# Kernel optimization log

Measured on AMD Instinct MI355X. Metric: run time of the kernel, lower is better.

Reference implementation:

```python
import jax, jax.numpy as jnp
import numpy as np

SIZE = 2.0            # scene extent, matches init size
N_LEVELS = 16         # Instant-NGP default
TABLE_SIZE = 1 << 19  # hash entries per level (power of 2)
FEAT = 2              # embedding_length per level
BASE_RES = 16         # init resolution
MAX_RES = 2048
N_POINTS = 1 << 21

_OFFS = np.array([[(c >> d) & 1 for d in range(3)] for c in range(8)])  # [8,3] corner bits
_PRIMES = np.array([1, 2654435761, 805459861], dtype=np.uint32)         # NGP spatial hash primes


def setup_inputs() -> dict:
    key = jax.random.key(0)
    k1, k2 = jax.random.split(key)
    xyz = (jax.random.uniform(k1, (N_POINTS, 3), dtype=jnp.float32) - 0.5) * SIZE
    tables = jax.random.normal(k2, (N_LEVELS, TABLE_SIZE, FEAT), dtype=jnp.float32) * 1e-2
    # geometric resolution schedule 16 -> 2048 over 16 levels
    growth = (MAX_RES / BASE_RES) ** (np.arange(N_LEVELS) / (N_LEVELS - 1))
    resolutions = jnp.asarray(np.floor(BASE_RES * growth).astype(np.int32))
    return {"xyz": xyz, "tables": tables, "resolutions": resolutions}


def _encode(xyz, tables, resolutions):
    u = xyz / SIZE + 0.5                              # [N,3] in [0,1)
    offs_u = jnp.asarray(_OFFS.astype(np.uint32))     # [8,3]
    offs_f = jnp.asarray(_OFFS.astype(np.float32))    # [8,3]
    primes = jnp.asarray(_PRIMES)

    def level(_, xs):
        table, res = xs                               # [T,F], scalar int32
        p = u * res.astype(jnp.float32)               # [N,3]
        p0 = jnp.floor(p)
        w = p - p0                                    # trilinear fractions [N,3]
        c = p0.astype(jnp.uint32)[:, None, :] + offs_u[None]     # [N,8,3]
        h = (c[..., 0] * primes[0]) ^ (c[..., 1] * primes[1]) ^ (c[..., 2] * primes[2])
        idx = (h & jnp.uint32(TABLE_SIZE - 1)).astype(jnp.int32)  # [N,8]
        feats = table[idx]                                        # [N,8,F] gather
        wc = jnp.prod(jnp.where(offs_f[None] > 0, w[:, None, :], 1.0 - w[:, None, :]), axis=-1)  # [N,8]
        return None, jnp.sum(feats * wc[..., None], axis=1)      # [N,F]

    _, embs = jax.lax.scan(level, None, (tables, resolutions))   # [L,N,F]
    n = xyz.shape[0]
    return jnp.transpose(embs, (1, 0, 2)).reshape(n, N_LEVELS * FEAT)


def reference(xyz, tables, resolutions):
    return _encode(xyz, tables, resolutions)
```

## Files before the change

### kernel.cpp

```cpp
#include <hip/hip_runtime.h>
#include <hip/hip_fp16.h>

#define NLV 16
#define TBL (1u << 19)
#define TMASK (TBL - 1u)
#define P1 2654435761u
#define P2 805459861u
#define NBIN (1 << 18)

typedef float vf2 __attribute__((ext_vector_type(2)));
typedef float vf4 __attribute__((ext_vector_type(4)));
typedef unsigned vu2 __attribute__((ext_vector_type(2)));

__device__ __forceinline__ vf2 h2_to_f2(unsigned bits) {
    union { unsigned u; __half2 h; } c; c.u = bits;
    float2 f = __half22float2(c.h);
    vf2 r; r.x = f.x; r.y = f.y; return r;
}
__device__ __forceinline__ unsigned f2_to_h2(float a, float b) {
    union { __half2 h; unsigned u; } c; c.h = __floats2half2_rn(a, b);
    return c.u;
}

__device__ __forceinline__ unsigned mort6(unsigned v) {
    v &= 63u;
    v = (v | (v << 16)) & 0x030000FFu;
    v = (v | (v << 8))  & 0x0300F00Fu;
    v = (v | (v << 4))  & 0x030C30C3u;
    v = (v | (v << 2))  & 0x09249249u;
    return v;
}

__device__ __forceinline__ unsigned bin_of(float ux, float uy, float uz) {
    unsigned bx = min(63u, (unsigned)(ux * 64.0f));
    unsigned by = min(63u, (unsigned)(uy * 64.0f));
    unsigned bz = min(63u, (unsigned)(uz * 64.0f));
    return mort6(bx) | (mort6(by) << 1) | (mort6(bz) << 2);
}

__global__ __launch_bounds__(256) void convert_tables(
    const float* __restrict__ tables, unsigned* __restrict__ htab, int total)
{
    int i = blockIdx.x * 256 + threadIdx.x;
    int e0 = i * 2;
    if (e0 >= total) return;
    vf4 v = *(const vf4*)(tables + (size_t)e0 * 2);
    vu2 o; o.x = f2_to_h2(v.x, v.y); o.y = f2_to_h2(v.z, v.w);
    *(vu2*)(htab + e0) = o;
}

__global__ __launch_bounds__(256) void hist_kernel(
    const float* __restrict__ xyz, unsigned* __restrict__ hist, int n)
{
    int p = blockIdx.x * 256 + threadIdx.x;
    if (p >= n) return;
    float ux = xyz[(size_t)p * 3 + 0] * 0.5f + 0.5f;
    float uy = xyz[(size_t)p * 3 + 1] * 0.5f + 0.5f;
    float uz = xyz[(size_t)p * 3 + 2] * 0.5f + 0.5f;
    atomicAdd(&hist[bin_of(ux, uy, uz)], 1u);
}

__global__ __launch_bounds__(1024) void scan_bins(unsigned* __restrict__ hist)
{
    __shared__ unsigned part[1024];
    int t = threadIdx.x;
    int base = t * (NBIN / 1024);
    unsigned s = 0;
    for (int j = 0; j < NBIN / 1024; ++j) s += hist[base + j];
    part[t] = s;
    __syncthreads();
    for (int off = 1; off < 1024; off <<= 1) {
        unsigned v = (t >= off) ? part[t - off] : 0u;
        __syncthreads();
        part[t] += v;
        __syncthreads();
    }
    unsigned run = (t == 0) ? 0u : part[t - 1];
    for (int j = 0; j < NBIN / 1024; ++j) {
        unsigned tmp = hist[base + j];
        hist[base + j] = run;
        run += tmp;
    }
}

__global__ __launch_bounds__(256) void scatter_kernel(
    const float* __restrict__ xyz, unsigned* __restrict__ start,
    vf4* __restrict__ u4s, int* __restrict__ orig, int n)
{
    int p = blockIdx.x * 256 + threadIdx.x;
    if (p >= n) return;
    float ux = xyz[(size_t)p * 3 + 0] * 0.5f + 0.5f;
    float uy = xyz[(size_t)p * 3 + 1] * 0.5f + 0.5f;
    float uz = xyz[(size_t)p * 3 + 2] * 0.5f + 0.5f;
    unsigned pos = atomicAdd(&start[bin_of(ux, uy, uz)], 1u);
    orig[pos] = p;
    vf4 r; r.x = ux; r.y = uy; r.z = uz; r.w = 0.0f;
    u4s[pos] = r;
}

__global__ __launch_bounds__(256) void ngp_gather_s(
    const vf4* __restrict__ u4s,
    const unsigned* __restrict__ htab,
    const int* __restrict__ resolutions,
    unsigned* __restrict__ wsout,
    int n, int nbPerLevel)
{
    int L = blockIdx.x / nbPerLevel;
    int chunk = blockIdx.x % nbPerLevel;
    int p0 = chunk * 1024 + (int)threadIdx.x;

    float res = (float)resolutions[L];
    const unsigned* __restrict__ tab = htab + (size_t)L * TBL;
    unsigned* __restrict__ wl = wsout + (size_t)L * n;

    unsigned idx[4][8];
    float wx[4], wyz[4][4];
    bool valid[4];

#pragma unroll
    for (int q = 0; q < 4; ++q) {
        int p = p0 + q * 256;
        valid[q] = (p < n);
        int pp = valid[q] ? p : 0;
        vf4 u = u4s[pp];
        float px = u.x * res, py = u.y * res, pz = u.z * res;
        float fx = floorf(px), fy = floorf(py), fz = floorf(pz);
        float wxl = px - fx, wyl = py - fy, wzl = pz - fz;
        unsigned cx = (unsigned)fx, cy = (unsigned)fy, cz = (unsigned)fz;
        unsigned hx0 = cx, hx1 = cx + 1u;
        unsigned hy0 = cy * P1, hy1 = hy0 + P1;
        unsigned hz0 = cz * P2, hz1 = hz0 + P2;
#pragma unroll
        for (int c = 0; c < 8; ++c)
            idx[q][c] = ((((c & 1) ? hx1 : hx0) ^
                          ((c & 2) ? hy1 : hy0) ^
                          ((c & 4) ? hz1 : hz0)) & TMASK);
        float vy = 1.0f - wyl, vz = 1.0f - wzl;
        wx[q] = wxl;
        wyz[q][0] = vy * vz;  wyz[q][1] = wyl * vz;
        wyz[q][2] = vy * wzl; wyz[q][3] = wyl * wzl;
    }

    unsigned d[4][8];
#pragma unroll
    for (int q = 0; q < 4; ++q)
#pragma unroll
        for (int c = 0; c < 8; ++c)
            d[q][c] = tab[idx[q][c]];

#pragma unroll
    for (int q = 0; q < 4; ++q) {
        float vx = 1.0f - wx[q];
        float a0 = 0.0f, a1 = 0.0f;
#pragma unroll
        for (int c = 0; c < 8; ++c) {
            float w = wyz[q][c >> 1] * ((c & 1) ? wx[q] : vx);
            vf2 f = h2_to_f2(d[q][c]);
            a0 += f.x * w;
            a1 += f.y * w;
        }
        int p = p0 + q * 256;
        if (valid[q]) wl[p] = f2_to_h2(a0, a1);
    }
}

__global__ __launch_bounds__(256) void ngp_finalize_s(
    const unsigned* __restrict__ ws, const int* __restrict__ orig,
    float* __restrict__ out, int n)
{
    int i = blockIdx.x * 256 + threadIdx.x;
    if (i >= n) return;
    int op = orig[i];
    vf4* o = (vf4*)(out + (size_t)op * (NLV * 2));
#pragma unroll
    for (int j = 0; j < 8; ++j) {
        vf2 ga = h2_to_f2(ws[(size_t)(2 * j) * n + i]);
        vf2 gb = h2_to_f2(ws[(size_t)(2 * j + 1) * n + i]);
        vf4 r; r.x = ga.x; r.y = ga.y; r.z = gb.x; r.w = gb.y;
        o[j] = r;
    }
}

__global__ __launch_bounds__(256) void ngp_encode_kernel(
    const float* __restrict__ xyz,
    const float* __restrict__ tables,
    const int* __restrict__ resolutions,
    float* __restrict__ out,
    int n)
{
    int p = blockIdx.x * blockDim.x + threadIdx.x;
    if (p >= n) return;

    float x = xyz[(size_t)p * 3 + 0];
    float y = xyz[(size_t)p * 3 + 1];
    float z = xyz[(size_t)p * 3 + 2];
    float ux = x * 0.5f + 0.5f;
    float uy = y * 0.5f + 0.5f;
    float uz = z * 0.5f + 0.5f;

    float acc[NLV * 2];

#pragma unroll
    for (int L = 0; L < NLV; ++L) {
        float res = (float)resolutions[L];
        float px = ux * res, py = uy * res, pz = uz * res;
        float fx = floorf(px), fy = floorf(py), fz = floorf(pz);
        float wx = px - fx, wy = py - fy, wz = pz - fz;
        unsigned cx = (unsigned)fx, cy = (unsigned)fy, cz = (unsigned)fz;
        unsigned hx0 = cx, hx1 = cx + 1u;
        unsigned hy0 = cy * P1, hy1 = hy0 + P1;
        unsigned hz0 = cz * P2, hz1 = hz0 + P2;
        const vf2* __restrict__ tab = (const vf2*)tables + (size_t)L * TBL;
        float vx = 1.0f - wx, vy = 1.0f - wy, vz = 1.0f - wz;
        float a0 = 0.0f, a1 = 0.0f;
#pragma unroll
        for (int c = 0; c < 8; ++c) {
            unsigned h = ((c & 1) ? hx1 : hx0) ^
                         ((c & 2) ? hy1 : hy0) ^
                         ((c & 4) ? hz1 : hz0);
            vf2 f = tab[h & TMASK];
            float w = ((c & 1) ? wx : vx) *
                      ((c & 2) ? wy : vy) *
                      ((c & 4) ? wz : vz);
            a0 += f.x * w;
            a1 += f.y * w;
        }
        acc[L * 2 + 0] = a0;
        acc[L * 2 + 1] = a1;
    }

    vf4* o = (vf4*)(out + (size_t)p * (NLV * 2));
#pragma unroll
    for (int i = 0; i < 8; ++i) {
        vf4 r; r.x = acc[i * 4 + 0]; r.y = acc[i * 4 + 1];
        r.z = acc[i * 4 + 2]; r.w = acc[i * 4 + 3];
        o[i] = r;
    }
}

extern "C" void kernel_launch(void* const* d_in, const int* in_sizes, int n_in,
                              void* d_out, int out_size, void* d_ws, size_t ws_size,
                              hipStream_t stream) {
    const float* xyz = (const float*)d_in[0];
    const float* tables = (const float*)d_in[1];
    const int* resolutions = (const int*)d_in[2];
    float* out = (float*)d_out;

    int n = in_sizes[0] / 3;
    const int totalEntries = NLV * (int)TBL;

    const size_t tabBytes  = (size_t)totalEntries * 4;
    const size_t u4Bytes   = (size_t)n * sizeof(vf4);
    const size_t origBytes = (size_t)n * 4;
    const size_t histBytes = (size_t)NBIN * 4;
    const size_t wsoutBytes = (size_t)NLV * (size_t)n * 4;
    const size_t need = tabBytes + u4Bytes + origBytes + histBytes + wsoutBytes;

    if (ws_size >= need) {
        char* base = (char*)d_ws;
        unsigned* htab  = (unsigned*)base;                       base += tabBytes;
        vf4*      u4s   = (vf4*)base;                            base += u4Bytes;
        int*      orig  = (int*)base;                            base += origBytes;
        unsigned* hist  = (unsigned*)base;                       base += histBytes;
        unsigned* wsout = (unsigned*)base;

        hipMemsetAsync(hist, 0, histBytes, stream);

        int gridC = (totalEntries / 2 + 255) / 256;
        hipLaunchKernelGGL(convert_tables, dim3(gridC), dim3(256), 0, stream,
                           tables, htab, totalEntries);

        int gridP = (n + 255) / 256;
        hipLaunchKernelGGL(hist_kernel, dim3(gridP), dim3(256), 0, stream,
                           xyz, hist, n);
        hipLaunchKernelGGL(scan_bins, dim3(1), dim3(1024), 0, stream, hist);
        hipLaunchKernelGGL(scatter_kernel, dim3(gridP), dim3(256), 0, stream,
                           xyz, hist, u4s, orig, n);

        int nbPerLevel = (n + 1023) / 1024;
        int grid1 = NLV * nbPerLevel;
        hipLaunchKernelGGL(ngp_gather_s, dim3(grid1), dim3(256), 0, stream,
                           u4s, htab, resolutions, wsout, n, nbPerLevel);

        hipLaunchKernelGGL(ngp_finalize_s, dim3(gridP), dim3(256), 0, stream,
                           wsout, orig, out, n);
    } else {
        int grid = (n + 255) / 256;
        hipLaunchKernelGGL(ngp_encode_kernel, dim3(grid), dim3(256), 0, stream,
                           xyz, tables, resolutions, out, n);
    }
}
```

Baseline: 884.2 us.

## Fuse per-level gather with finalize, coarsen Morton bins, vectorize hist/scatter

Replaces the level-major gather kernel plus separate finalize pass with one point-major kernel that walks all 16 levels, two at a time, per point and writes the output row directly. This drops the fp16 intermediate workspace and its write/read round trip. Morton sort bins shrink from 64^3 to 32^3, and the histogram and scatter kernels now process four points per thread using vector loads. The trade-off is that fine levels no longer get level-major scheduling, so table locality in cache may be worse.

```diff
diff --git a/kernel.cpp b/kernel.cpp
--- a/kernel.cpp
+++ b/kernel.cpp
@@ -6,7 +6,7 @@
 #define TMASK (TBL - 1u)
 #define P1 2654435761u
 #define P2 805459861u
-#define NBIN (1 << 18)
+#define NBIN (1 << 15)
 
 typedef float vf2 __attribute__((ext_vector_type(2)));
 typedef float vf4 __attribute__((ext_vector_type(4)));
@@ -22,8 +22,8 @@
     return c.u;
 }
 
-__device__ __forceinline__ unsigned mort6(unsigned v) {
-    v &= 63u;
+__device__ __forceinline__ unsigned mort5(unsigned v) {
+    v &= 31u;
     v = (v | (v << 16)) & 0x030000FFu;
     v = (v | (v << 8))  & 0x0300F00Fu;
     v = (v | (v << 4))  & 0x030C30C3u;
@@ -32,10 +32,10 @@
 }
 
 __device__ __forceinline__ unsigned bin_of(float ux, float uy, float uz) {
-    unsigned bx = min(63u, (unsigned)(ux * 64.0f));
-    unsigned by = min(63u, (unsigned)(uy * 64.0f));
-    unsigned bz = min(63u, (unsigned)(uz * 64.0f));
-    return mort6(bx) | (mort6(by) << 1) | (mort6(bz) << 2);
+    unsigned bx = min(31u, (unsigned)(ux * 32.0f));
+    unsigned by = min(31u, (unsigned)(uy * 32.0f));
+    unsigned bz = min(31u, (unsigned)(uz * 32.0f));
+    return mort5(bx) | (mort5(by) << 1) | (mort5(bz) << 2);
 }
 
 __global__ __launch_bounds__(256) void convert_tables(
@@ -52,12 +52,25 @@
 __global__ __launch_bounds__(256) void hist_kernel(
     const float* __restrict__ xyz, unsigned* __restrict__ hist, int n)
 {
-    int p = blockIdx.x * 256 + threadIdx.x;
+    int t = blockIdx.x * 256 + threadIdx.x;
+    int p = t * 4;
     if (p >= n) return;
-    float ux = xyz[(size_t)p * 3 + 0] * 0.5f + 0.5f;
-    float uy = xyz[(size_t)p * 3 + 1] * 0.5f + 0.5f;
-    float uz = xyz[(size_t)p * 3 + 2] * 0.5f + 0.5f;
-    atomicAdd(&hist[bin_of(ux, uy, uz)], 1u);
+    if (p + 3 < n) {
+        vf4 a = *(const vf4*)(xyz + (size_t)p * 3);
+        vf4 b = *(const vf4*)(xyz + (size_t)p * 3 + 4);
+        vf4 c = *(const vf4*)(xyz + (size_t)p * 3 + 8);
+        atomicAdd(&hist[bin_of(a.x*0.5f+0.5f, a.y*0.5f+0.5f, a.z*0.5f+0.5f)], 1u);
+        atomicAdd(&hist[bin_of(a.w*0.5f+0.5f, b.x*0.5f+0.5f, b.y*0.5f+0.5f)], 1u);
+        atomicAdd(&hist[bin_of(b.z*0.5f+0.5f, b.w*0.5f+0.5f, c.x*0.5f+0.5f)], 1u);
+        atomicAdd(&hist[bin_of(c.y*0.5f+0.5f, c.z*0.5f+0.5f, c.w*0.5f+0.5f)], 1u);
+    } else {
+        for (int q = 0; q < 4 && p + q < n; ++q) {
+            float ux = xyz[(size_t)(p+q)*3+0]*0.5f+0.5f;
+            float uy = xyz[(size_t)(p+q)*3+1]*0.5f+0.5f;
+            float uz = xyz[(size_t)(p+q)*3+2]*0.5f+0.5f;
+            atomicAdd(&hist[bin_of(ux,uy,uz)], 1u);
+        }
+    }
 }
 
 __global__ __launch_bounds__(1024) void scan_bins(unsigned* __restrict__ hist)
@@ -87,96 +100,108 @@
     const float* __restrict__ xyz, unsigned* __restrict__ start,
     vf4* __restrict__ u4s, int* __restrict__ orig, int n)
 {
-    int p = blockIdx.x * 256 + threadIdx.x;
+    int t = blockIdx.x * 256 + threadIdx.x;
+    int p = t * 4;
     if (p >= n) return;
-    float ux = xyz[(size_t)p * 3 + 0] * 0.5f + 0.5f;
-    float uy = xyz[(size_t)p * 3 + 1] * 0.5f + 0.5f;
-    float uz = xyz[(size_t)p * 3 + 2] * 0.5f + 0.5f;
-    unsigned pos = atomicAdd(&start[bin_of(ux, uy, uz)], 1u);
-    orig[pos] = p;
-    vf4 r; r.x = ux; r.y = uy; r.z = uz; r.w = 0.0f;
-    u4s[pos] = r;
-}
-
-__global__ __launch_bounds__(256) void ngp_gather_s(
+    float U[4][3];
+    int cnt = (p + 3 < n) ? 4 : (n - p);
+    if (cnt == 4) {
+        vf4 a = *(const vf4*)(xyz + (size_t)p * 3);
+        vf4 b = *(const vf4*)(xyz + (size_t)p * 3 + 4);
+        vf4 c = *(const vf4*)(xyz + (size_t)p * 3 + 8);
+        U[0][0]=a.x; U[0][1]=a.y; U[0][2]=a.z;
+        U[1][0]=a.w; U[1][1]=b.x; U[1][2]=b.y;
+        U[2][0]=b.z; U[2][1]=b.w; U[2][2]=c.x;
+        U[3][0]=c.y; U[3][1]=c.z; U[3][2]=c.w;
+    } else {
+        for (int q = 0; q < cnt; ++q) {
+            U[q][0]=xyz[(size_t)(p+q)*3+0];
+            U[q][1]=xyz[(size_t)(p+q)*3+1];
+            U[q][2]=xyz[(size_t)(p+q)*3+2];
+        }
+    }
+#pragma unroll
+    for (int q = 0; q < 4; ++q) {
+        if (q >= cnt) break;
+        float ux = U[q][0]*0.5f+0.5f, uy = U[q][1]*0.5f+0.5f, uz = U[q][2]*0.5f+0.5f;
+        unsigned pos = atomicAdd(&start[bin_of(ux,uy,uz)], 1u);
+        orig[pos] = p + q;
+        vf4 r; r.x = ux; r.y = uy; r.z = uz; r.w = 0.0f;
+        u4s[pos] = r;
+    }
+}
+
+__global__ __launch_bounds__(256) void ngp_fused(
     const vf4* __restrict__ u4s,
     const unsigned* __restrict__ htab,
     const int* __restrict__ resolutions,
-    unsigned* __restrict__ wsout,
-    int n, int nbPerLevel)
-{
-    int L = blockIdx.x / nbPerLevel;
-    int chunk = blockIdx.x % nbPerLevel;
-    int p0 = chunk * 1024 + (int)threadIdx.x;
-
-    float res = (float)resolutions[L];
-    const unsigned* __restrict__ tab = htab + (size_t)L * TBL;
-    unsigned* __restrict__ wl = wsout + (size_t)L * n;
-
-    unsigned idx[4][8];
-    float wx[4], wyz[4][4];
-    bool valid[4];
-
-#pragma unroll
-    for (int q = 0; q < 4; ++q) {
-        int p = p0 + q * 256;
-        valid[q] = (p < n);
-        int pp = valid[q] ? p : 0;
-        vf4 u = u4s[pp];
-        float px = u.x * res, py = u.y * res, pz = u.z * res;
-        float fx = floorf(px), fy = floorf(py), fz = floorf(pz);
-        float wxl = px - fx, wyl = py - fy, wzl = pz - fz;
-        unsigned cx = (unsigned)fx, cy = (unsigned)fy, cz = (unsigned)fz;
-        unsigned hx0 = cx, hx1 = cx + 1u;
-        unsigned hy0 = cy * P1, hy1 = hy0 + P1;
-        unsigned hz0 = cz * P2, hz1 = hz0 + P2;
-#pragma unroll
-        for (int c = 0; c < 8; ++c)
-            idx[q][c] = ((((c & 1) ? hx1 : hx0) ^
-                          ((c & 2) ? hy1 : hy0) ^
-                          ((c & 4) ? hz1 : hz0)) & TMASK);
-        float vy = 1.0f - wyl, vz = 1.0f - wzl;
-        wx[q] = wxl;
-        wyz[q][0] = vy * vz;  wyz[q][1] = wyl * vz;
-        wyz[q][2] = vy * wzl; wyz[q][3] = wyl * wzl;
-    }
-
-    unsigned d[4][8];
-#pragma unroll
-    for (int q = 0; q < 4; ++q)
-#pragma unroll
-        for (int c = 0; c < 8; ++c)
-            d[q][c] = tab[idx[q][c]];
-
-#pragma unroll
-    for (int q = 0; q < 4; ++q) {
-        float vx = 1.0f - wx[q];
-        float a0 = 0.0f, a1 = 0.0f;
-#pragma unroll
-        for (int c = 0; c < 8; ++c) {
-            float w = wyz[q][c >> 1] * ((c & 1) ? wx[q] : vx);
-            vf2 f = h2_to_f2(d[q][c]);
-            a0 += f.x * w;
-            a1 += f.y * w;
-        }
-        int p = p0 + q * 256;
-        if (valid[q]) wl[p] = f2_to_h2(a0, a1);
-    }
-}
-
-__global__ __launch_bounds__(256) void ngp_finalize_s(
-    const unsigned* __restrict__ ws, const int* __restrict__ orig,
+    const int* __restrict__ orig,
     float* __restrict__ out, int n)
 {
     int i = blockIdx.x * 256 + threadIdx.x;
     if (i >= n) return;
+
+    vf4 u = u4s[i];
     int op = orig[i];
+
+    float acc[NLV * 2];
+
+#pragma unroll
+    for (int Lp = 0; Lp < NLV / 2; ++Lp) {
+        unsigned idx[2][8];
+        float wxs[2], wyz[2][4];
+#pragma unroll
+        for (int s = 0; s < 2; ++s) {
+            int L = 2 * Lp + s;
+            float res = (float)resolutions[L];
+            float px = u.x * res, py = u.y * res, pz = u.z * res;
+            float fx = floorf(px), fy = floorf(py), fz = floorf(pz);
+            float wxl = px - fx, wyl = py - fy, wzl = pz - fz;
+            unsigned cx = (unsigned)fx, cy = (unsigned)fy, cz = (unsigned)fz;
+            unsigned hx0 = cx, hx1 = cx + 1u;
+            unsigned hy0 = cy * P1, hy1 = hy0 + P1;
+            unsigned hz0 = cz * P2, hz1 = hz0 + P2;
+#pragma unroll
+            for (int c = 0; c < 8; ++c)
+                idx[s][c] = ((((c & 1) ? hx1 : hx0) ^
+                              ((c & 2) ? hy1 : hy0) ^
+                              ((c & 4) ? hz1 : hz0)) & TMASK);
+            float vy = 1.0f - wyl, vz = 1.0f - wzl;
+            wxs[s] = wxl;
+            wyz[s][0] = vy * vz;  wyz[s][1] = wyl * vz;
+            wyz[s][2] = vy * wzl; wyz[s][3] = wyl * wzl;
+        }
+
+        unsigned d[2][8];
+#pragma unroll
+        for (int s = 0; s < 2; ++s) {
+            const unsigned* __restrict__ tab = htab + (size_t)(2 * Lp + s) * TBL;
+#pragma unroll
+            for (int c = 0; c < 8; ++c)
+                d[s][c] = tab[idx[s][c]];
+        }
+
+#pragma unroll
+        for (int s = 0; s < 2; ++s) {
+            float vx = 1.0f - wxs[s];
+            float a0 = 0.0f, a1 = 0.0f;
+#pragma unroll
+            for (int c = 0; c < 8; ++c) {
+                float w = wyz[s][c >> 1] * ((c & 1) ? wxs[s] : vx);
+                vf2 f = h2_to_f2(d[s][c]);
+                a0 += f.x * w;
+                a1 += f.y * w;
+            }
+            acc[(2 * Lp + s) * 2 + 0] = a0;
+            acc[(2 * Lp + s) * 2 + 1] = a1;
+        }
+    }
+
     vf4* o = (vf4*)(out + (size_t)op * (NLV * 2));
 #pragma unroll
     for (int j = 0; j < 8; ++j) {
-        vf2 ga = h2_to_f2(ws[(size_t)(2 * j) * n + i]);
-        vf2 gb = h2_to_f2(ws[(size_t)(2 * j + 1) * n + i]);
-        vf4 r; r.x = ga.x; r.y = ga.y; r.z = gb.x; r.w = gb.y;
+        vf4 r; r.x = acc[j * 4 + 0]; r.y = acc[j * 4 + 1];
+        r.z = acc[j * 4 + 2]; r.w = acc[j * 4 + 3];
         o[j] = r;
     }
 }
@@ -253,16 +278,14 @@
     const size_t u4Bytes   = (size_t)n * sizeof(vf4);
     const size_t origBytes = (size_t)n * 4;
     const size_t histBytes = (size_t)NBIN * 4;
-    const size_t wsoutBytes = (size_t)NLV * (size_t)n * 4;
-    const size_t need = tabBytes + u4Bytes + origBytes + histBytes + wsoutBytes;
+    const size_t need = tabBytes + u4Bytes + origBytes + histBytes;
 
     if (ws_size >= need) {
         char* base = (char*)d_ws;
         unsigned* htab  = (unsigned*)base;                       base += tabBytes;
         vf4*      u4s   = (vf4*)base;                            base += u4Bytes;
         int*      orig  = (int*)base;                            base += origBytes;
-        unsigned* hist  = (unsigned*)base;                       base += histBytes;
-        unsigned* wsout = (unsigned*)base;
+        unsigned* hist  = (unsigned*)base;
 
         hipMemsetAsync(hist, 0, histBytes, stream);
 
@@ -270,20 +293,16 @@
         hipLaunchKernelGGL(convert_tables, dim3(gridC), dim3(256), 0, stream,
                            tables, htab, totalEntries);
 
-        int gridP = (n + 255) / 256;
-        hipLaunchKernelGGL(hist_kernel, dim3(gridP), dim3(256), 0, stream,
+        int grid4 = ((n + 3) / 4 + 255) / 256;
+        hipLaunchKernelGGL(hist_kernel, dim3(grid4), dim3(256), 0, stream,
                            xyz, hist, n);
         hipLaunchKernelGGL(scan_bins, dim3(1), dim3(1024), 0, stream, hist);
-        hipLaunchKernelGGL(scatter_kernel, dim3(gridP), dim3(256), 0, stream,
+        hipLaunchKernelGGL(scatter_kernel, dim3(grid4), dim3(256), 0, stream,
                            xyz, hist, u4s, orig, n);
 
-        int nbPerLevel = (n + 1023) / 1024;
-        int grid1 = NLV * nbPerLevel;
-        hipLaunchKernelGGL(ngp_gather_s, dim3(grid1), dim3(256), 0, stream,
-                           u4s, htab, resolutions, wsout, n, nbPerLevel);
-
-        hipLaunchKernelGGL(ngp_finalize_s, dim3(gridP), dim3(256), 0, stream,
-                           wsout, orig, out, n);
+        int gridP = (n + 255) / 256;
+        hipLaunchKernelGGL(ngp_fused, dim3(gridP), dim3(256), 0, stream,
+                           u4s, htab, resolutions, orig, out, n);
     } else {
         int grid = (n + 255) / 256;
         hipLaunchKernelGGL(ngp_encode_kernel, dim3(grid), dim3(256), 0, stream,
```

Result: slower. 922.2 us (+4.3%).
